# Performance work log

Measured on AMD Instinct MI355X. Metric: run time of the kernel, lower is better.

Reference implementation:

```python
import jax, jax.numpy as jnp
import numpy as np

NUM_NODES = 50000
D_IN = 256
D_OUT = 256
N_QUERIES = 128
PER_GROUP = 256            # edges per query group in the last step (> max_edges)
E1 = N_QUERIES * PER_GROUP # 32768
E0 = 32768
RATIO = 0.2                # ratio_update


def setup_inputs() -> dict:
    key = jax.random.key(0)
    ks = jax.random.split(key, 10)
    d4 = 4 * D_IN
    rng = np.random.default_rng(0)
    # last-step edges: col0 = query idx (sorted, equal-size groups), col6 = src, col7 = dst
    edges1 = np.zeros((E1, 8), np.int64)
    edges1[:, 0] = np.repeat(np.arange(N_QUERIES), PER_GROUP)
    edges1[:, 6] = rng.integers(0, NUM_NODES, E1)
    edges1[:, 7] = rng.integers(0, NUM_NODES, E1)
    # earlier-step edges
    edges0 = np.zeros((E0, 8), np.int64)
    edges0[:, 0] = rng.integers(0, N_QUERIES, E0)
    edges0[:, 6] = rng.integers(0, NUM_NODES, E0)
    edges0[:, 7] = rng.integers(0, NUM_NODES, E0)
    return {
        "visited_node_score": jax.random.uniform(ks[0], (NUM_NODES,), jnp.float32),
        "visited_node_representation": jax.random.normal(ks[1], (NUM_NODES, D_IN), jnp.float32),
        "selected_edges0": jnp.asarray(edges0),
        "selected_edges1": jnp.asarray(edges1),
        "rel_emb0": jax.random.normal(ks[2], (E0, D_IN), jnp.float32),
        "rel_emb1": jax.random.normal(ks[3], (E1, D_IN), jnp.float32),
        "query_src_ts_emb": jax.random.normal(ks[4], (N_QUERIES, D_IN), jnp.float32),
        "query_rel_emb": jax.random.normal(ks[5], (N_QUERIES, D_IN), jnp.float32),
        "Wq": jax.random.normal(ks[6], (d4, d4), jnp.float32) * np.sqrt(2.0 / d4),
        "Wk": jax.random.normal(ks[7], (d4, d4), jnp.float32) * np.sqrt(2.0 / d4),
        "Wl": jax.random.normal(ks[8], (D_OUT, D_IN), jnp.float32) * np.sqrt(2.0 / (D_IN + D_OUT)),
        "bl": jnp.zeros((D_OUT,), jnp.float32),
        "max_edges": 64,
    }


def _att_score(edges, node_repr, rel, qst_tab, qr_tab, Wq, Wk):
    # G3: sum(Q(cat(vi,rel,qst,qr)) * K(cat(vj,rel,qst,qr)), -1) per edge
    q, src, dst = edges[:, 0], edges[:, 6], edges[:, 7]
    qst, qr = qst_tab[q], qr_tab[q]
    left = jnp.concatenate([node_repr[src], rel, qst, qr], axis=-1)   # [E, 4d]
    right = jnp.concatenate([node_repr[dst], rel, qst, qr], axis=-1)  # [E, 4d]
    return jnp.sum((left @ Wq.T) * (right @ Wk.T), axis=-1)          # [E]


def _seg_softmax(logits, seg, n):
    m = jax.ops.segment_max(logits, seg, num_segments=n)
    e = jnp.exp(logits - m[seg])
    s = jax.ops.segment_sum(e, seg, num_segments=n)
    return e / s[seg]


def _update_repr(edges, node_repr, w, ratio):
    # sparse mm: out[src] += (1-ratio)*w_e*repr[dst]; + identity for non-src rows, + ratio*repr for src rows
    src, dst = edges[:, 6], edges[:, 7]
    n = node_repr.shape[0]
    agg = jax.ops.segment_sum(((1.0 - ratio) * w)[:, None] * node_repr[dst], src, num_segments=n)
    is_src = jnp.zeros((n,), bool).at[src].set(True)
    diag = jnp.where(is_src, ratio, 1.0)
    return agg + diag[:, None] * node_repr


def reference(visited_node_score, visited_node_representation, selected_edges0,
              selected_edges1, rel_emb0, rel_emb1, query_src_ts_emb, query_rel_emb,
              Wq, Wk, Wl, bl, max_edges):
    n = visited_node_representation.shape[0]
    nq = query_src_ts_emb.shape[0]
    pg = selected_edges1.shape[0] // nq
    # attention on last step's edges
    logits = _att_score(selected_edges1, visited_node_representation, rel_emb1,
                        query_src_ts_emb, query_rel_emb, Wq, Wk)
    src1 = selected_edges1[:, 6]
    src_score = visited_node_score[src1]
    soft = _seg_softmax(logits, src1, n)
    target = soft * src_score
    # per-query-group top-k pruning (each group has pg > k edges)
    _, ti = jax.lax.top_k(target.reshape(nq, pg), max_edges)  # [nq, k]
    orig_indices = (ti + (jnp.arange(nq) * pg)[:, None]).reshape(-1)
    pruned_edges = selected_edges1[orig_indices]
    pruned_src_score = src_score[orig_indices]
    pruned_soft = soft[orig_indices]
    # sparse scatter-aggregation of scores onto dst (col 7)
    updated_node_score = jax.ops.segment_sum(pruned_soft * pruned_src_score,
                                             pruned_edges[:, 7], num_segments=n)
    node_repr = _update_repr(pruned_edges, visited_node_representation, pruned_soft, RATIO)
    # back-propagate representations through the earlier step
    tl = _att_score(selected_edges0, node_repr, rel_emb0, query_src_ts_emb, query_rel_emb, Wq, Wk)
    ts = _seg_softmax(tl, selected_edges0[:, 6], n)
    node_repr = _update_repr(selected_edges0, node_repr, ts, RATIO)
    # bypass_forward: LeakyReLU(Linear(.))
    node_repr = jax.nn.leaky_relu(node_repr @ Wl.T + bl)
    return (updated_node_score, node_repr, pruned_edges, orig_indices)
```

## Files before the change

### kernel.cpp

```cpp
#include <hip/hip_runtime.h>

#define NN 50000
#define D 256
#define NQ 128
#define PG 256
#define NE 32768
#define ME 64
#define BCAP 32
#define KDIM 256
#define NKT 8

typedef _Float16 f16;
typedef __attribute__((ext_vector_type(4))) _Float16 f16x4;
typedef __attribute__((ext_vector_type(8))) _Float16 f16x8;
typedef __attribute__((ext_vector_type(4))) float f32x4;

#define MFMA16(a,b,c) __builtin_amdgcn_mfma_f32_16x16x32_f16(a,b,c,0,0,0)

__device__ __forceinline__ unsigned fenc(float f){
  unsigned b = __float_as_uint(f);
  return (b & 0x80000000u) ? ~b : (b | 0x80000000u);
}
__device__ __forceinline__ float fdec(unsigned u){
  unsigned b = (u & 0x80000000u) ? (u & 0x7fffffffu) : ~u;
  return __uint_as_float(b);
}
__device__ __forceinline__ void split8(float4 a, float4 b, f16x8& h, f16x8& l){
  float v[8] = {a.x,a.y,a.z,a.w,b.x,b.y,b.z,b.w};
#pragma unroll
  for (int i=0;i<8;++i){
    _Float16 hh = (_Float16)v[i];
    h[i] = hh;
    l[i] = (_Float16)(v[i] - (float)hh);
  }
}

template<int EPI>
__global__ __launch_bounds__(256) void hgemm(const float* __restrict__ A,
                                             int Mrows,
                                             const f16* __restrict__ Bh, const f16* __restrict__ Bl,
                                             float* __restrict__ C, int ldc,
                                             const float* __restrict__ bias)
{
  __shared__ f16 AsH[128*40], AsL[128*40], BsH[128*40], BsL[128*40];
  const int tid = threadIdx.x;
  const int rb = blockIdx.x*128, cb = blockIdx.y*128;
  const int row = tid >> 1, ko = (tid & 1)*16;
  const bool aok = (rb + row) < Mrows;
  const int lane = tid & 63, wv = tid >> 6;
  const int qrw = (wv & 1)*64, qcw = (wv >> 1)*64;
  const int lm = lane & 15, qd = lane >> 4;

  const float* gA = A + (size_t)(rb+row)*KDIM + ko;
  const f16* gBh = Bh + (size_t)(cb+row)*KDIM + ko;
  const f16* gBl = Bl + (size_t)(cb+row)*KDIM + ko;

  float4 pa0=make_float4(0.f,0.f,0.f,0.f), pa1=pa0, pa2=pa0, pa3=pa0;
  f16x8 pbh0, pbh1, pbl0, pbl1;
  if (aok){ pa0 = *(const float4*)gA;     pa1 = *(const float4*)(gA+4);
            pa2 = *(const float4*)(gA+8); pa3 = *(const float4*)(gA+12); }
  pbh0 = *(const f16x8*)gBh; pbh1 = *(const f16x8*)(gBh+8);
  pbl0 = *(const f16x8*)gBl; pbl1 = *(const f16x8*)(gBl+8);

  f32x4 acc[4][4];
#pragma unroll
  for (int t=0;t<4;++t)
#pragma unroll
    for (int u=0;u<4;++u)
#pragma unroll
      for (int r=0;r<4;++r) acc[t][u][r] = 0.f;

  const int wbase = row*40 + ko;
  for (int kt = 0; kt < NKT; ++kt){
    __syncthreads();
    {
      f16x8 h0,h1,l0,l1;
      split8(pa0,pa1,h0,l0); split8(pa2,pa3,h1,l1);
      *(f16x8*)(AsH + wbase) = h0; *(f16x8*)(AsH + wbase + 8) = h1;
      *(f16x8*)(AsL + wbase) = l0; *(f16x8*)(AsL + wbase + 8) = l1;
      *(f16x8*)(BsH + wbase) = pbh0; *(f16x8*)(BsH + wbase + 8) = pbh1;
      *(f16x8*)(BsL + wbase) = pbl0; *(f16x8*)(BsL + wbase + 8) = pbl1;
    }
    __syncthreads();
    if (kt+1 < NKT){
      const int k0 = (kt+1)*32;
      if (aok){ pa0 = *(const float4*)(gA + k0);     pa1 = *(const float4*)(gA + k0 + 4);
                pa2 = *(const float4*)(gA + k0 + 8); pa3 = *(const float4*)(gA + k0 + 12); }
      pbh0 = *(const f16x8*)(gBh + k0); pbh1 = *(const f16x8*)(gBh + k0 + 8);
      pbl0 = *(const f16x8*)(gBl + k0); pbl1 = *(const f16x8*)(gBl + k0 + 8);
    }
    f16x8 fah[4], fal[4], fbh[4], fbl[4];
#pragma unroll
    for (int t=0;t<4;++t){
      int off = (qrw + t*16 + lm)*40 + qd*8;
      fah[t] = *(const f16x8*)(AsH + off);
      fal[t] = *(const f16x8*)(AsL + off);
    }
#pragma unroll
    for (int u=0;u<4;++u){
      int off = (qcw + u*16 + lm)*40 + qd*8;
      fbh[u] = *(const f16x8*)(BsH + off);
      fbl[u] = *(const f16x8*)(BsL + off);
    }
#pragma unroll
    for (int t=0;t<4;++t)
#pragma unroll
      for (int u=0;u<4;++u){
        acc[t][u] = MFMA16(fah[t], fbh[u], acc[t][u]);
        acc[t][u] = MFMA16(fah[t], fbl[u], acc[t][u]);
        acc[t][u] = MFMA16(fal[t], fbh[u], acc[t][u]);
      }
  }
#pragma unroll
  for (int t=0;t<4;++t){
#pragma unroll
    for (int u=0;u<4;++u){
      int col = cb + qcw + u*16 + lm;
      f32x4 v = acc[t][u];
#pragma unroll
      for (int r=0;r<4;++r){
        int rg = rb + qrw + t*16 + qd*4 + r;
        if (rg < Mrows){
          float x = v[r];
          if (EPI==1){ x += bias[col]; x = x > 0.f ? x : 0.01f*x; }
          C[(size_t)rg*ldc + col] = x;
        }
      }
    }
  }
}

__global__ __launch_bounds__(256) void hgemm_rel(const float* __restrict__ A,
                                                 const f16* __restrict__ Bh, const f16* __restrict__ Bl,
                                                 const int* __restrict__ edges,
                                                 const float* __restrict__ H,
                                                 const float* __restrict__ Rel,
                                                 float* __restrict__ logits)
{
  __shared__ f16 AsH[128*40], AsL[128*40], BsH[128*40], BsL[128*40];
  __shared__ int sIdx[128];
  const int tid = threadIdx.x;
  const int rb = blockIdx.x*128, cb = blockIdx.y*128;
  const int sec = blockIdx.y >> 1;
  const int row = tid >> 1, ko = (tid & 1)*16;
  const int lane = tid & 63, wv = tid >> 6;
  const int qrw = (wv & 1)*64, qcw = (wv >> 1)*64;
  const int lm = lane & 15, qd = lane >> 4;

  if (tid < 128){
    int e = rb + tid;
    sIdx[tid] = (sec==0) ? edges[(size_t)e*8+6] : (sec==1 ? edges[(size_t)e*8+7] : 0);
  }

  const float* gA = A + (size_t)(rb+row)*KDIM + ko;
  const f16* gBh = Bh + (size_t)(cb+row)*KDIM + ko;
  const f16* gBl = Bl + (size_t)(cb+row)*KDIM + ko;

  float4 pa0 = *(const float4*)gA,     pa1 = *(const float4*)(gA+4);
  float4 pa2 = *(const float4*)(gA+8), pa3 = *(const float4*)(gA+12);
  f16x8 pbh0 = *(const f16x8*)gBh, pbh1 = *(const f16x8*)(gBh+8);
  f16x8 pbl0 = *(const f16x8*)gBl, pbl1 = *(const f16x8*)(gBl+8);

  f32x4 acc[4][4];
#pragma unroll
  for (int t=0;t<4;++t)
#pragma unroll
    for (int u=0;u<4;++u)
#pragma unroll
      for (int r=0;r<4;++r) acc[t][u][r] = 0.f;

  const int wbase = row*40 + ko;
  for (int kt = 0; kt < NKT; ++kt){
    __syncthreads();
    {
      f16x8 h0,h1,l0,l1;
      split8(pa0,pa1,h0,l0); split8(pa2,pa3,h1,l1);
      *(f16x8*)(AsH + wbase) = h0; *(f16x8*)(AsH + wbase + 8) = h1;
      *(f16x8*)(AsL + wbase) = l0; *(f16x8*)(AsL + wbase + 8) = l1;
      *(f16x8*)(BsH + wbase) = pbh0; *(f16x8*)(BsH + wbase + 8) = pbh1;
      *(f16x8*)(BsL + wbase) = pbl0; *(f16x8*)(BsL + wbase + 8) = pbl1;
    }
    __syncthreads();
    if (kt+1 < NKT){
      const int k0 = (kt+1)*32;
      pa0 = *(const float4*)(gA + k0);     pa1 = *(const float4*)(gA + k0 + 4);
      pa2 = *(const float4*)(gA + k0 + 8); pa3 = *(const float4*)(gA + k0 + 12);
      pbh0 = *(const f16x8*)(gBh + k0); pbh1 = *(const f16x8*)(gBh + k0 + 8);
      pbl0 = *(const f16x8*)(gBl + k0); pbl1 = *(const f16x8*)(gBl + k0 + 8);
    }
    f16x8 fah[4], fal[4], fbh[4], fbl[4];
#pragma unroll
    for (int t=0;t<4;++t){
      int off = (qrw + t*16 + lm)*40 + qd*8;
      fah[t] = *(const f16x8*)(AsH + off);
      fal[t] = *(const f16x8*)(AsL + off);
    }
#pragma unroll
    for (int u=0;u<4;++u){
      int off = (qcw + u*16 + lm)*40 + qd*8;
      fbh[u] = *(const f16x8*)(BsH + off);
      fbl[u] = *(const f16x8*)(BsL + off);
    }
#pragma unroll
    for (int t=0;t<4;++t)
#pragma unroll
      for (int u=0;u<4;++u){
        acc[t][u] = MFMA16(fah[t], fbh[u], acc[t][u]);
        acc[t][u] = MFMA16(fah[t], fbl[u], acc[t][u]);
        acc[t][u] = MFMA16(fal[t], fbh[u], acc[t][u]);
      }
  }
  const int cbase = ((blockIdx.y & 1)*128) + qcw + lm;
#pragma unroll
  for (int t=0;t<4;++t){
#pragma unroll
    for (int r=0;r<4;++r){
      int lrow = qrw + t*16 + qd*4 + r;
      int e = rb + lrow;
      const float* xb = (sec==2) ? (Rel + (size_t)e*256)
                                 : (H + (size_t)sIdx[lrow]*256);
      float p = acc[t][0][r]*xb[cbase]
              + acc[t][1][r]*xb[cbase+16]
              + acc[t][2][r]*xb[cbase+32]
              + acc[t][3][r]*xb[cbase+48];
      p += __shfl_xor(p, 1); p += __shfl_xor(p, 2);
      p += __shfl_xor(p, 4); p += __shfl_xor(p, 8);
      if (lm == 0) atomicAdd(logits + e, p);
    }
  }
}

__global__ void split_f16(const float* __restrict__ X, f16* __restrict__ Xh,
                          f16* __restrict__ Xl, int n)
{
  int i = (blockIdx.x*256 + threadIdx.x)*4;
  if (i >= n) return;
  float4 v = *(const float4*)(X+i);
  f16x4 h, l;
  h[0]=(_Float16)v.x; h[1]=(_Float16)v.y; h[2]=(_Float16)v.z; h[3]=(_Float16)v.w;
  l[0]=(_Float16)(v.x-(float)h[0]); l[1]=(_Float16)(v.y-(float)h[1]);
  l[2]=(_Float16)(v.z-(float)h[2]); l[3]=(_Float16)(v.w-(float)h[3]);
  *(f16x4*)(Xh+i)=h; *(f16x4*)(Xl+i)=l;
}

__global__ void build_bt_mhh(const float* __restrict__ M, f16* __restrict__ Bh, f16* __restrict__ Bl)
{
  int idx = blockIdx.x*256 + threadIdx.x;
  int n = idx >> 8, k = idx & 255;
  float v = M[(size_t)k*1024 + n];
  _Float16 h = (_Float16)v;
  Bh[idx] = h; Bl[idx] = (_Float16)(v - (float)h);
}

__global__ void build_bt_wcat(const float* __restrict__ M, f16* __restrict__ Bh, f16* __restrict__ Bl)
{
  int idx = blockIdx.x*256 + threadIdx.x;
  int j = idx >> 8, k = idx & 255;
  float v;
  if (j < 256)      v = M[(size_t)j*1024 + 256 + k];
  else if (j < 512) v = M[(size_t)(256+k)*1024 + (j-256)];
  else              v = M[(size_t)(256 + j-512)*1024 + 256 + k];
  _Float16 h = (_Float16)v;
  Bh[idx] = h; Bl[idx] = (_Float16)(v - (float)h);
}

__global__ __launch_bounds__(256) void gemm_tn_split(const float* __restrict__ A,
                                                     const float* __restrict__ B,
                                                     double* __restrict__ Cpart)
{
  __shared__ float As[16][68];
  __shared__ float Bs[16][68];
  const int tid = threadIdx.x;
  const int rb = blockIdx.x * 64, cb = blockIdx.y * 64;
  const int z  = blockIdx.z;
  const int ty = tid >> 4, tx = tid & 15;
  const int aj = tid >> 4, akk = (tid & 15) << 2;
  double acc[4][4] = {};
  const int jbeg = z * 128, jend = jbeg + 128;
  for (int j0 = jbeg; j0 < jend; j0 += 16) {
    float4 av = *(const float4*)(A + (size_t)(j0+aj)*1024 + rb + akk);
    As[aj][akk+0]=av.x; As[aj][akk+1]=av.y; As[aj][akk+2]=av.z; As[aj][akk+3]=av.w;
    float4 bv = *(const float4*)(B + (size_t)(j0+aj)*1024 + cb + akk);
    Bs[aj][akk+0]=bv.x; Bs[aj][akk+1]=bv.y; Bs[aj][akk+2]=bv.z; Bs[aj][akk+3]=bv.w;
    __syncthreads();
#pragma unroll
    for (int jj=0; jj<16; ++jj){
      float a0=As[jj][ty*4+0],a1=As[jj][ty*4+1],a2=As[jj][ty*4+2],a3=As[jj][ty*4+3];
      float b0=Bs[jj][tx*4+0],b1=Bs[jj][tx*4+1],b2=Bs[jj][tx*4+2],b3=Bs[jj][tx*4+3];
      acc[0][0]+=(double)a0*b0; acc[0][1]+=(double)a0*b1; acc[0][2]+=(double)a0*b2; acc[0][3]+=(double)a0*b3;
      acc[1][0]+=(double)a1*b0; acc[1][1]+=(double)a1*b1; acc[1][2]+=(double)a1*b2; acc[1][3]+=(double)a1*b3;
      acc[2][0]+=(double)a2*b0; acc[2][1]+=(double)a2*b1; acc[2][2]+=(double)a2*b2; acc[2][3]+=(double)a2*b3;
      acc[3][0]+=(double)a3*b0; acc[3][1]+=(double)a3*b1; acc[3][2]+=(double)a3*b2; acc[3][3]+=(double)a3*b3;
    }
    __syncthreads();
  }
  double* Cz = Cpart + (size_t)z * 1048576;
#pragma unroll
  for (int i=0;i<4;++i)
#pragma unroll
    for (int j=0;j<4;++j)
      Cz[(size_t)(rb+ty*4+i)*1024 + cb+tx*4+j] = acc[i][j];
}

__global__ void reduce_m(const double* __restrict__ P, float* __restrict__ Mout)
{
  int i = blockIdx.x*256 + threadIdx.x;
  double s = 0.0;
#pragma unroll
  for (int z=0;z<8;++z) s += P[(size_t)i + (size_t)z*1048576];
  Mout[i] = (float)s;
}

__global__ void build_g(const float* __restrict__ qst, const float* __restrict__ qr,
                        float* __restrict__ G)
{
  int idx = blockIdx.x*256 + threadIdx.x;
  int q = idx >> 9, k = idx & 511;
  G[idx] = (k < 256) ? qst[(size_t)q*256 + k] : qr[(size_t)q*256 + k - 256];
}

__global__ void build_bq(const float* __restrict__ M, float* __restrict__ Bq)
{
  int idx = blockIdx.x*256 + threadIdx.x;
  int k = idx / 1280, t = idx - k*1280;
  float v;
  if (t < 256)      v = M[(size_t)t*1024 + 512 + k];
  else if (t < 512) v = M[(size_t)(512+k)*1024 + (t-256)];
  else if (t < 768) v = M[(size_t)(256+(t-512))*1024 + 512 + k]
                      + M[(size_t)(512+k)*1024 + 256 + (t-512)];
  else              v = M[(size_t)(512+k)*1024 + 512 + (t-768)];
  Bq[idx] = v;
}

__global__ __launch_bounds__(256) void gemm64(const float* __restrict__ A, int lda,
                                              const float* __restrict__ B, int ldb,
                                              float* __restrict__ C, int ldc,
                                              int Mrows, int Kdim)
{
  __shared__ float As[16][68];
  __shared__ float Bs[16][68];
  const int tid = threadIdx.x;
  const int rb = blockIdx.x*64, cb = blockIdx.y*64;
  const int tx = tid & 15, ty = tid >> 4;
  const int a_r = tid >> 2, a_k = (tid & 3)*4;
  const int b_c = tid & 63, b_r0 = (tid >> 6)*4;
  const bool aok = (rb + a_r) < Mrows;
  float4 pa = make_float4(0.f,0.f,0.f,0.f);
  float pb[4];
  if (aok) pa = *(const float4*)(A + (size_t)(rb+a_r)*lda + a_k);
#pragma unroll
  for (int j=0;j<4;++j) pb[j] = B[(size_t)(b_r0+j)*ldb + cb + b_c];
  float acc[4][4] = {};
  const int NK = Kdim >> 4;
  for (int t0=0; t0<NK; ++t0){
    __syncthreads();
    As[a_k+0][a_r]=pa.x; As[a_k+1][a_r]=pa.y; As[a_k+2][a_r]=pa.z; As[a_k+3][a_r]=pa.w;
#pragma unroll
    for (int j=0;j<4;++j) Bs[b_r0+j][b_c] = pb[j];
    __syncthreads();
    if (t0+1 < NK){
      int k0 = (t0+1) << 4;
      if (aok) pa = *(const float4*)(A + (size_t)(rb+a_r)*lda + k0 + a_k);
#pragma unroll
      for (int j=0;j<4;++j) pb[j] = B[(size_t)(k0+b_r0+j)*ldb + cb + b_c];
    }
#pragma unroll
    for (int kk=0;kk<16;++kk){
      float a[4], b[4];
      *(float4*)&a[0] = *(const float4*)&As[kk][ty*4];
#pragma unroll
      for (int j=0;j<4;++j) b[j] = Bs[kk][tx + 16*j];
#pragma unroll
      for (int i=0;i<4;++i)
#pragma unroll
        for (int j=0;j<4;++j) acc[i][j] += a[i]*b[j];
    }
  }
#pragma unroll
  for (int i=0;i<4;++i){
    int r = rb + ty*4 + i;
    if (r < Mrows)
#pragma unroll
      for (int j=0;j<4;++j)
        C[(size_t)r*ldc + cb + tx + 16*j] = acc[i][j];
  }
}

__global__ __launch_bounds__(256) void qc_dot(const float* __restrict__ Ccat,
    const float* __restrict__ qst, const float* __restrict__ qr, float* __restrict__ qc)
{
  __shared__ float red[256];
  int q = blockIdx.x, t = threadIdx.x;
  float a = Ccat[(size_t)q*1280 + 768 + t]  * qst[(size_t)q*256 + t]
          + Ccat[(size_t)q*1280 + 1024 + t] * qr [(size_t)q*256 + t];
  red[t] = a;
  __syncthreads();
  for (int s=128; s>0; s>>=1){
    if (t < s) red[t] += red[t+s];
    __syncthreads();
  }
  if (t==0) qc[q] = red[0];
}

__global__ __launch_bounds__(256) void slim_logits(const int* __restrict__ edges,
    const float* __restrict__ H, const float* __restrict__ U,
    const float* __restrict__ Rel,
    const float* __restrict__ Ct, const float* __restrict__ qc,
    float* __restrict__ logits)
{
  int lane = threadIdx.x & 63;
  int e = blockIdx.x*4 + (threadIdx.x >> 6);
  int q   = edges[(size_t)e*8 + 0];
  int src = edges[(size_t)e*8 + 6];
  int dst = edges[(size_t)e*8 + 7];
  const float4* hs = (const float4*)(H   + (size_t)src*256);
  const float4* hd = (const float4*)(H   + (size_t)dst*256);
  const float4* us = (const float4*)(U   + (size_t)src*256);
  const float4* rl = (const float4*)(Rel + (size_t)e*256);
  const float4* t1 = (const float4*)(Ct + (size_t)q*1280);
  const float4* t2 = (const float4*)(Ct + (size_t)q*1280 + 256);
  const float4* w4 = (const float4*)(Ct + (size_t)q*1280 + 512);
  float4 a, b, c;
  float s = 0.f;
  a = hd[lane]; b = us[lane]; c = t2[lane];
  s += a.x*(b.x+c.x) + a.y*(b.y+c.y) + a.z*(b.z+c.z) + a.w*(b.w+c.w);
  a = hs[lane]; c = t1[lane];
  s += a.x*c.x + a.y*c.y + a.z*c.z + a.w*c.w;
  a = rl[lane]; c = w4[lane];
  s += a.x*c.x + a.y*c.y + a.z*c.z + a.w*c.w;
#pragma unroll
  for (int off=32; off>0; off>>=1) s += __shfl_down(s, off);
  if (lane==0) logits[e] = s + qc[q];
}

__global__ void segmax_k(const int* __restrict__ edges, const float* __restrict__ logits,
                         unsigned* __restrict__ menc, int nE)
{
  int e = blockIdx.x*256 + threadIdx.x; if (e >= nE) return;
  atomicMax(menc + edges[(size_t)e*8+6], fenc(logits[e]));
}
__global__ void segexp_k(const int* __restrict__ edges, const float* __restrict__ logits,
                         const unsigned* __restrict__ menc, float* __restrict__ ebuf,
                         float* __restrict__ ssum, int nE)
{
  int e = blockIdx.x*256 + threadIdx.x; if (e >= nE) return;
  int s = edges[(size_t)e*8+6];
  float ex = expf(logits[e] - fdec(menc[s]));
  ebuf[e] = ex;
  atomicAdd(ssum + s, ex);
}
template<int TGT>
__global__ void segsoft_k(const int* __restrict__ edges, const float* __restrict__ ebuf,
                          const float* __restrict__ ssum, float* __restrict__ soft,
                          const float* __restrict__ score, float* __restrict__ target, int nE)
{
  int e = blockIdx.x*256 + threadIdx.x; if (e >= nE) return;
  int s = edges[(size_t)e*8+6];
  float so = ebuf[e] / ssum[s];
  soft[e] = so;
  if (TGT) target[e] = so * score[s];
}

__global__ __launch_bounds__(256) void topk_k(const float* __restrict__ target,
    const float* __restrict__ soft, const int* __restrict__ edges1,
    float* __restrict__ out0, float* __restrict__ out2, float* __restrict__ out3,
    int* __restrict__ p_src, int* __restrict__ p_dst, float* __restrict__ p_w)
{
  int qb = blockIdx.x, t = threadIdx.x;
  __shared__ float v[256];
  __shared__ int   ix[256];
  v[t] = target[(size_t)qb*256 + t];
  ix[t] = t;
  __syncthreads();
  for (int k=2; k<=256; k<<=1){
    for (int j=k>>1; j>0; j>>=1){
      int ixj = t ^ j;
      if (ixj > t){
        float va=v[t], vb=v[ixj]; int ia=ix[t], ib=ix[ixj];
        bool dir  = ((t & k) == 0);
        bool l_ab = (va > vb) || (va == vb && ia < ib);
        bool sw   = dir ? (!l_ab) : l_ab;
        if (sw){ v[t]=vb; v[ixj]=va; ix[t]=ib; ix[ixj]=ia; }
      }
      __syncthreads();
    }
  }
  if (t < 64){
    int oi = qb*256 + ix[t];
    int o  = qb*64 + t;
    out3[o] = (float)oi;
#pragma unroll
    for (int c2=0;c2<8;++c2) out2[(size_t)o*8 + c2] = (float)edges1[(size_t)oi*8 + c2];
    int s_ = edges1[(size_t)oi*8+6], d_ = edges1[(size_t)oi*8+7];
    p_src[o] = s_; p_dst[o] = d_; p_w[o] = soft[oi];
    atomicAdd(out0 + d_, v[t]);
  }
}

__global__ void bucket_fill(const int* __restrict__ srcarr, int stride, int n,
                            int* __restrict__ counts, int* __restrict__ bucket,
                            int* __restrict__ over, int* __restrict__ n_over)
{
  int e = blockIdx.x*256 + threadIdx.x; if (e >= n) return;
  int s = srcarr[(size_t)e*stride];
  int pos = atomicAdd(counts + s, 1);
  if (pos < BCAP) bucket[(size_t)s*BCAP + pos] = e;
  else { int oi = atomicAdd(n_over, 1); over[oi] = e; }
}

__global__ __launch_bounds__(256) void fused_update(const int* __restrict__ counts,
    const int* __restrict__ bucket, const int* __restrict__ dstarr, int dstride,
    const float* __restrict__ w, const float* __restrict__ Hin, float* __restrict__ Hout)
{
  int lane = threadIdx.x & 63;
  int n = blockIdx.x*4 + (threadIdx.x >> 6);
  if (n >= NN) return;
  int cnt = counts[n];
  float fac = cnt > 0 ? 0.2f : 1.0f;
  float4 h = ((const float4*)(Hin + (size_t)n*256))[lane];
  float4 acc = make_float4(fac*h.x, fac*h.y, fac*h.z, fac*h.w);
  int m = cnt < BCAP ? cnt : BCAP;
  for (int i=0;i<m;++i){
    int e = bucket[(size_t)n*BCAP + i];
    int d = dstarr[(size_t)e*dstride];
    float f = 0.8f * w[e];
    float4 vv = ((const float4*)(Hin + (size_t)d*256))[lane];
    acc.x += f*vv.x; acc.y += f*vv.y; acc.z += f*vv.z; acc.w += f*vv.w;
  }
  ((float4*)(Hout + (size_t)n*256))[lane] = acc;
}

__global__ __launch_bounds__(256) void over_k(const int* __restrict__ over,
    const int* __restrict__ n_over,
    const int* __restrict__ srcarr, int sstride,
    const int* __restrict__ dstarr, int dstride,
    const float* __restrict__ w, const float* __restrict__ Hin, float* __restrict__ Hout)
{
  int lane = threadIdx.x & 63;
  int i = blockIdx.x*4 + (threadIdx.x >> 6);
  if (i >= *n_over) return;
  int e = over[i];
  int s = srcarr[(size_t)e*sstride], d = dstarr[(size_t)e*dstride];
  float f = 0.8f * w[e];
  float4 vv = ((const float4*)(Hin + (size_t)d*256))[lane];
  float* o = Hout + (size_t)s*256 + lane*4;
  atomicAdd(o+0, f*vv.x); atomicAdd(o+1, f*vv.y);
  atomicAdd(o+2, f*vv.z); atomicAdd(o+3, f*vv.w);
}

extern "C" void kernel_launch(void* const* d_in, const int* in_sizes, int n_in,
                              void* d_out, int out_size, void* d_ws, size_t ws_size,
                              hipStream_t stream)
{
  const float* score = (const float*)d_in[0];
  const float* H0    = (const float*)d_in[1];
  const int*   edges0= (const int*)d_in[2];
  const int*   edges1= (const int*)d_in[3];
  const float* rel0  = (const float*)d_in[4];
  const float* rel1  = (const float*)d_in[5];
  const float* qst   = (const float*)d_in[6];
  const float* qr    = (const float*)d_in[7];
  const float* Wq    = (const float*)d_in[8];
  const float* Wk    = (const float*)d_in[9];
  const float* Wl    = (const float*)d_in[10];
  const float* bl    = (const float*)d_in[11];
  (void)in_sizes; (void)n_in; (void)out_size; (void)ws_size;

  float* out0 = (float*)d_out;
  float* out1 = out0 + NN;
  float* out2 = out1 + (size_t)NN*D;
  float* out3 = out2 + (size_t)NQ*ME*8;

  float* ws     = (float*)d_ws;
  float* Mbuf   = ws;
  float* Ccat   = ws + 1048576;
  float* qcv    = ws + 1212416;
  float* G      = ws + 1212544;
  float* logits = ws + 1278080;
  float* ebuf   = ws + 1310848;
  float* soft   = ws + 1343616;
  float* target = ws + 1376384;
  unsigned* menc= (unsigned*)(ws + 1409152);
  float* ssum   = ws + 1459152;
  int* p_src    = (int*)(ws + 1509152);
  int* p_dst    = (int*)(ws + 1517344);
  float* p_w    = ws + 1525536;
  float* Bq     = ws + 1533728;
  float* U      = ws + 2189088;
  float* Hnew   = ws + 14989088;
  float* SCR    = ws + 27789088;
  int* counts = (int*)SCR;
  int* n_over = (int*)(SCR + 50000);
  int* over   = (int*)(SCR + 50056);
  int* bucket = (int*)(SCR + 100000);
  float* P0   = SCR + 2000000;
  double* Mpart = (double*)P0;
  f16* mhh_h  = (f16*)P0;
  f16* mhh_l  = (f16*)(P0 + 32768);
  f16* wcat_h = (f16*)(P0 + 65536);
  f16* wcat_l = (f16*)(P0 + 163840);
  f16* wl_h   = (f16*)(P0 + 262144);
  f16* wl_l   = (f16*)(P0 + 294912);
  float* Hpre = U;

  hipMemsetAsync(out0, 0, (size_t)NN*4, stream);
  hipMemsetAsync(menc, 0, (size_t)NN*4, stream);
  hipMemsetAsync(ssum, 0, (size_t)NN*4, stream);

  gemm_tn_split<<<dim3(16,16,8), 256, 0, stream>>>(Wq, Wk, Mpart);
  reduce_m<<<4096, 256, 0, stream>>>(Mpart, Mbuf);
  build_g<<<256, 256, 0, stream>>>(qst, qr, G);
  build_bq<<<2560, 256, 0, stream>>>(Mbuf, Bq);
  gemm64<<<dim3(2,20), 256, 0, stream>>>(G, 512, Bq, 1280, Ccat, 1280, NQ, 512);
  qc_dot<<<NQ, 256, 0, stream>>>(Ccat, qst, qr, qcv);
  build_bt_mhh<<<256, 256, 0, stream>>>(Mbuf, mhh_h, mhh_l);
  build_bt_wcat<<<768, 256, 0, stream>>>(Mbuf, wcat_h, wcat_l);
  split_f16<<<64, 256, 0, stream>>>(Wl, wl_h, wl_l, 65536);

  hgemm<0><<<dim3(391,2), 256, 0, stream>>>(H0, NN, mhh_h, mhh_l, U, 256, nullptr);
  slim_logits<<<NE/4, 256, 0, stream>>>(edges1, H0, U, rel1, Ccat, qcv, logits);
  hgemm_rel<<<dim3(256,6), 256, 0, stream>>>(rel1, wcat_h, wcat_l, edges1, H0, rel1, logits);

  segmax_k<<<NE/256, 256, 0, stream>>>(edges1, logits, menc, NE);
  segexp_k<<<NE/256, 256, 0, stream>>>(edges1, logits, menc, ebuf, ssum, NE);
  segsoft_k<1><<<NE/256, 256, 0, stream>>>(edges1, ebuf, ssum, soft, score, target, NE);

  topk_k<<<NQ, 256, 0, stream>>>(target, soft, edges1, out0, out2, out3, p_src, p_dst, p_w);

  hipMemsetAsync(counts, 0, (size_t)NN*4, stream);
  hipMemsetAsync(n_over, 0, 4, stream);
  bucket_fill<<<(NQ*ME+255)/256, 256, 0, stream>>>(p_src, 1, NQ*ME, counts, bucket, over, n_over);
  fused_update<<<(NN+3)/4, 256, 0, stream>>>(counts, bucket, p_dst, 1, p_w, H0, Hnew);
  over_k<<<(NQ*ME)/4, 256, 0, stream>>>(over, n_over, p_src, 1, p_dst, 1, p_w, H0, Hnew);

  hipMemsetAsync(menc, 0, (size_t)NN*4, stream);
  hipMemsetAsync(ssum, 0, (size_t)NN*4, stream);

  hgemm<0><<<dim3(391,2), 256, 0, stream>>>(Hnew, NN, mhh_h, mhh_l, U, 256, nullptr);
  slim_logits<<<NE/4, 256, 0, stream>>>(edges0, Hnew, U, rel0, Ccat, qcv, logits);
  hgemm_rel<<<dim3(256,6), 256, 0, stream>>>(rel0, wcat_h, wcat_l, edges0, Hnew, rel0, logits);

  segmax_k<<<NE/256, 256, 0, stream>>>(edges0, logits, menc, NE);
  segexp_k<<<NE/256, 256, 0, stream>>>(edges0, logits, menc, ebuf, ssum, NE);
  segsoft_k<0><<<NE/256, 256, 0, stream>>>(edges0, ebuf, ssum, soft, nullptr, nullptr, NE);

  hipMemsetAsync(counts, 0, (size_t)NN*4, stream);
  hipMemsetAsync(n_over, 0, 4, stream);
  bucket_fill<<<NE/256, 256, 0, stream>>>(edges0 + 6, 8, NE, counts, bucket, over, n_over);
  fused_update<<<(NN+3)/4, 256, 0, stream>>>(counts, bucket, edges0 + 7, 8, soft, Hnew, Hpre);
  over_k<<<NE/4, 256, 0, stream>>>(over, n_over, edges0 + 6, 8, edges0 + 7, 8, soft, Hnew, Hpre);

  hgemm<1><<<dim3(391,2), 256, 0, stream>>>(Hpre, NN, wl_h, wl_l, out1, 256, bl);
}
```

Measured before the change: 607.9 us.

## Enlarge FP64 Wq^T·Wk GEMM tiles to 128x128 with register prefetch

The split-K double-precision GEMM that forms Wq^T·Wk now computes 128x128 output tiles with 8x8 per-thread accumulators instead of 64x64 with 4x4. Shared tiles are stored as doubles with padded strides and read as double2 vectors. Global loads for the next K-slice are issued into registers before the current slice is computed, which overlaps memory latency with FMAs. The grid shrinks to 8x8x8 blocks, trading occupancy and higher register pressure (64 double accumulators per thread) for more reuse per shared-memory load.

After: 615.2 us. About the same (+1.2%).

```diff
diff --git a/kernel.cpp b/kernel.cpp
--- a/kernel.cpp
+++ b/kernel.cpp
@@ -268,38 +268,70 @@
                                                      const float* __restrict__ B,
                                                      double* __restrict__ Cpart)
 {
-  __shared__ float As[16][68];
-  __shared__ float Bs[16][68];
+  __shared__ __align__(16) double As[16*162];
+  __shared__ __align__(16) double Bs[16*162];
   const int tid = threadIdx.x;
-  const int rb = blockIdx.x * 64, cb = blockIdx.y * 64;
+  const int rb = blockIdx.x * 128, cb = blockIdx.y * 128;
   const int z  = blockIdx.z;
   const int ty = tid >> 4, tx = tid & 15;
-  const int aj = tid >> 4, akk = (tid & 15) << 2;
-  double acc[4][4] = {};
-  const int jbeg = z * 128, jend = jbeg + 128;
-  for (int j0 = jbeg; j0 < jend; j0 += 16) {
-    float4 av = *(const float4*)(A + (size_t)(j0+aj)*1024 + rb + akk);
-    As[aj][akk+0]=av.x; As[aj][akk+1]=av.y; As[aj][akk+2]=av.z; As[aj][akk+3]=av.w;
-    float4 bv = *(const float4*)(B + (size_t)(j0+aj)*1024 + cb + akk);
-    Bs[aj][akk+0]=bv.x; Bs[aj][akk+1]=bv.y; Bs[aj][akk+2]=bv.z; Bs[aj][akk+3]=bv.w;
-    __syncthreads();
+  const int aj = tid >> 4, ag = tid & 15;
+  double acc[8][8] = {};
+  const int jbeg = z * 128;
+
+  const float* gA = A + (size_t)(jbeg+aj)*1024 + rb + ag*8;
+  const float* gB = B + (size_t)(jbeg+aj)*1024 + cb + ag*8;
+  float4 av0 = *(const float4*)gA, av1 = *(const float4*)(gA+4);
+  float4 bv0 = *(const float4*)gB, bv1 = *(const float4*)(gB+4);
+
+  const int wbase = aj*162 + ag*10;
+  for (int t0 = 0; t0 < 8; ++t0) {
+    __syncthreads();
+    {
+      double2* wa = (double2*)(As + wbase);
+      double2* wb = (double2*)(Bs + wbase);
+      wa[0] = make_double2((double)av0.x, (double)av0.y);
+      wa[1] = make_double2((double)av0.z, (double)av0.w);
+      wa[2] = make_double2((double)av1.x, (double)av1.y);
+      wa[3] = make_double2((double)av1.z, (double)av1.w);
+      wb[0] = make_double2((double)bv0.x, (double)bv0.y);
+      wb[1] = make_double2((double)bv0.z, (double)bv0.w);
+      wb[2] = make_double2((double)bv1.x, (double)bv1.y);
+      wb[3] = make_double2((double)bv1.z, (double)bv1.w);
+    }
+    __syncthreads();
+    if (t0 < 7){
+      gA += 16*1024; gB += 16*1024;
+      av0 = *(const float4*)gA; av1 = *(const float4*)(gA+4);
+      bv0 = *(const float4*)gB; bv1 = *(const float4*)(gB+4);
+    }
 #pragma unroll
     for (int jj=0; jj<16; ++jj){
-      float a0=As[jj][ty*4+0],a1=As[jj][ty*4+1],a2=As[jj][ty*4+2],a3=As[jj][ty*4+3];
-      float b0=Bs[jj][tx*4+0],b1=Bs[jj][tx*4+1],b2=Bs[jj][tx*4+2],b3=Bs[jj][tx*4+3];
-      acc[0][0]+=(double)a0*b0; acc[0][1]+=(double)a0*b1; acc[0][2]+=(double)a0*b2; acc[0][3]+=(double)a0*b3;
-      acc[1][0]+=(double)a1*b0; acc[1][1]+=(double)a1*b1; acc[1][2]+=(double)a1*b2; acc[1][3]+=(double)a1*b3;
-      acc[2][0]+=(double)a2*b0; acc[2][1]+=(double)a2*b1; acc[2][2]+=(double)a2*b2; acc[2][3]+=(double)a2*b3;
-      acc[3][0]+=(double)a3*b0; acc[3][1]+=(double)a3*b1; acc[3][2]+=(double)a3*b2; acc[3][3]+=(double)a3*b3;
-    }
-    __syncthreads();
+      const double* pa = As + jj*162 + ty*10;
+      const double* pb = Bs + jj*162 + tx*10;
+      double a[8], b[8];
+      *(double2*)&a[0] = *(const double2*)(pa);
+      *(double2*)&a[2] = *(const double2*)(pa+2);
+      *(double2*)&a[4] = *(const double2*)(pa+4);
+      *(double2*)&a[6] = *(const double2*)(pa+6);
+      *(double2*)&b[0] = *(const double2*)(pb);
+      *(double2*)&b[2] = *(const double2*)(pb+2);
+      *(double2*)&b[4] = *(const double2*)(pb+4);
+      *(double2*)&b[6] = *(const double2*)(pb+6);
+#pragma unroll
+      for (int i=0;i<8;++i)
+#pragma unroll
+        for (int j=0;j<8;++j)
+          acc[i][j] += a[i]*b[j];
+    }
   }
   double* Cz = Cpart + (size_t)z * 1048576;
 #pragma unroll
-  for (int i=0;i<4;++i)
-#pragma unroll
-    for (int j=0;j<4;++j)
-      Cz[(size_t)(rb+ty*4+i)*1024 + cb+tx*4+j] = acc[i][j];
+  for (int i=0;i<8;++i){
+    double* cr = Cz + (size_t)(rb+ty*8+i)*1024 + cb + tx*8;
+#pragma unroll
+    for (int j=0;j<8;j+=2)
+      *(double2*)(cr + j) = make_double2(acc[i][j], acc[i][j+1]);
+  }
 }
 
 __global__ void reduce_m(const double* __restrict__ P, float* __restrict__ Mout)
@@ -607,7 +639,7 @@
   hipMemsetAsync(menc, 0, (size_t)NN*4, stream);
   hipMemsetAsync(ssum, 0, (size_t)NN*4, stream);
 
-  gemm_tn_split<<<dim3(16,16,8), 256, 0, stream>>>(Wq, Wk, Mpart);
+  gemm_tn_split<<<dim3(8,8,8), 256, 0, stream>>>(Wq, Wk, Mpart);
   reduce_m<<<4096, 256, 0, stream>>>(Mpart, Mbuf);
   build_g<<<256, 256, 0, stream>>>(qst, qr, G);
   build_bq<<<2560, 256, 0, stream>>>(Mbuf, Bq);
```
